# Optimization experiments

Measured on AMD Instinct MI355X. Metric: run time of the kernel, lower is better.

Reference implementation:

```python
import jax, jax.numpy as jnp
from jax import lax
import numpy as np

EPS = 1e-06


def _box_filter(x, radius):
    # Depthwise box mean with zero padding (matches F.conv2d padding=radius),
    # implemented separably: O(r) per pixel instead of O(r^2).
    C = x.shape[1]
    k = 2 * radius + 1
    dn = ('NCHW', 'OIHW', 'NCHW')
    kern_h = jnp.ones((C, 1, k, 1), x.dtype)
    kern_w = jnp.ones((C, 1, 1, k), x.dtype) / (k * k)
    y = lax.conv_general_dilated(x, kern_h, (1, 1), [(radius, radius), (0, 0)],
                                 feature_group_count=C, dimension_numbers=dn)
    return lax.conv_general_dilated(y, kern_w, (1, 1), [(0, 0), (radius, radius)],
                                    feature_group_count=C, dimension_numbers=dn)


def setup_inputs() -> dict:
    key = jax.random.key(0)
    k1, k2 = jax.random.split(key)
    I = jax.random.uniform(k1, (8, 1, 1024, 1024), dtype=jnp.float32)
    p = jax.random.uniform(k2, (8, 3, 1024, 1024), dtype=jnp.float32)
    return {"I": I, "p": p, "radius": 3}


def reference(I, p, radius):
    mean_I = _box_filter(I, radius)            # (B,1,H,W)
    mean_p = _box_filter(p, radius)            # (B,3,H,W)
    mean_Ip = _box_filter(I * p, radius)
    mean_II = _box_filter(I * I, radius)
    cov_Ip = mean_Ip - mean_I * mean_p
    var_I = mean_II - mean_I * mean_I
    a = cov_Ip / (var_I + EPS)
    b = mean_p - a * mean_I
    mean_a = _box_filter(a, radius)
    mean_b = _box_filter(b, radius)
    q = mean_a * I + mean_b
    return jnp.clip(q, 0.0, 1.0)
```

## Files before the change

kernel.cpp:

```cpp
#include <hip/hip_runtime.h>


#define TPB   128
#define OUTW  116
#define SEGH  64
#define HW    1024
#define GW    134
#define EPSF  1e-6f
#define INV49 (1.0f/49.0f)

struct GFState {
    float4 rr[8];
    float ra0[8], rb0[8], ra1[8], rb1[8], ra2[8], rb2[8];
    float sI, sII, sp0, sp1, sp2, sq0, sq1, sq2;
    float t6a0, t6b0, t6a1, t6b1, t6a2, t6b2;
    float4 cur[4];
};

template<int JB>
__device__ __forceinline__ void halfStep(
    GFState& S, int j0, int Yb, int x_in, bool xok, int xc, int tid,
    const float* __restrict__ Ip, const float* __restrict__ P0,
    const float* __restrict__ P1, const float* __restrict__ P2,
    float* __restrict__ Q0, float* __restrict__ Q1, float* __restrict__ Q2,
    float4 (*cs8A)[GW], float4 (*cs8B)[GW],
    float4 (*cs6A)[GW], float2 (*cs6B)[GW],
    bool dostore, bool dopref)
{
    float Io[4];
    #pragma unroll
    for (int u = 0; u < 4; ++u) Io[u] = S.rr[(JB+u+2)&7].x;

    #pragma unroll
    for (int u = 0; u < 4; ++u) {
        const float4 c = S.cur[u];
        const float4 o = S.rr[(JB+u+1)&7];
        S.sI  += c.x - o.x;
        S.sII += c.x*c.x - o.x*o.x;
        S.sp0 += c.y - o.y;  S.sq0 += c.x*c.y - o.x*o.y;
        S.sp1 += c.z - o.z;  S.sq1 += c.x*c.z - o.x*o.z;
        S.sp2 += c.w - o.w;  S.sq2 += c.x*c.w - o.x*o.w;
        S.rr[(JB+u)&7] = c;
        cs8A[(JB+u)&3][tid+3] = make_float4(S.sI,  S.sII, S.sp0, S.sp1);
        cs8B[(JB+u)&3][tid+3] = make_float4(S.sp2, S.sq0, S.sq1, S.sq2);
    }
    __syncthreads();

    #pragma unroll
    for (int u = 0; u < 4; ++u) {
        const int ls = (JB+u)&3;
        float4 A = make_float4(0.f,0.f,0.f,0.f);
        float4 B = make_float4(0.f,0.f,0.f,0.f);
        #pragma unroll
        for (int d = 0; d < 7; ++d) {
            float4 a = cs8A[ls][tid+d];
            float4 b = cs8B[ls][tid+d];
            A.x += a.x; A.y += a.y; A.z += a.z; A.w += a.w;
            B.x += b.x; B.y += b.y; B.z += b.z; B.w += b.w;
        }
        const int  yc   = Yb + j0 + u - 3;
        const bool abok = xok && ((unsigned)yc < HW);
        const float mi  = A.x*INV49, mii = A.y*INV49;
        const float rv  = __builtin_amdgcn_rcpf(mii - mi*mi + EPSF);
        float a0,b0,a1,b1,a2,b2, mp, mq, a, b;
        mp = A.z*INV49; mq = B.y*INV49;
        a = (mq - mi*mp)*rv; b = fmaf(-a, mi, mp);
        a0 = abok ? a : 0.f; b0 = abok ? b : 0.f;
        mp = A.w*INV49; mq = B.z*INV49;
        a = (mq - mi*mp)*rv; b = fmaf(-a, mi, mp);
        a1 = abok ? a : 0.f; b1 = abok ? b : 0.f;
        mp = B.x*INV49; mq = B.w*INV49;
        a = (mq - mi*mp)*rv; b = fmaf(-a, mi, mp);
        a2 = abok ? a : 0.f; b2 = abok ? b : 0.f;

        const int as = (JB+u)&7, al = (JB+u+1)&7;
        S.t6a0 += a0 - S.ra0[al]; S.ra0[as] = a0;
        S.t6b0 += b0 - S.rb0[al]; S.rb0[as] = b0;
        S.t6a1 += a1 - S.ra1[al]; S.ra1[as] = a1;
        S.t6b1 += b1 - S.rb1[al]; S.rb1[as] = b1;
        S.t6a2 += a2 - S.ra2[al]; S.ra2[as] = a2;
        S.t6b2 += b2 - S.rb2[al]; S.rb2[as] = b2;
        cs6A[ls][tid+3] = make_float4(S.t6a0, S.t6b0, S.t6a1, S.t6b1);
        cs6B[ls][tid+3] = make_float2(S.t6a2, S.t6b2);
    }
    __syncthreads();

    if (dopref) {
        #pragma unroll
        for (int u = 0; u < 4; ++u) {
            const int y  = Yb + j0 + 4 + u;
            const bool ok = xok && ((unsigned)y < HW);
            const int yy = min(max(y, 0), HW-1);
            const size_t off = (size_t)yy*HW + xc;
            float v0 = Ip[off], v1 = P0[off], v2 = P1[off], v3 = P2[off];
            float4 v;
            v.x = ok ? v0 : 0.f; v.y = ok ? v1 : 0.f;
            v.z = ok ? v2 : 0.f; v.w = ok ? v3 : 0.f;
            S.cur[u] = v;
        }
    }

    if (dostore) {
        const bool sok = (tid >= 6) && (tid < 122) && (x_in < HW);
        #pragma unroll
        for (int u = 0; u < 4; ++u) {
            const int ls = (JB+u)&3;
            float4 A6 = make_float4(0.f,0.f,0.f,0.f);
            float2 B6 = make_float2(0.f,0.f);
            #pragma unroll
            for (int d = 0; d < 7; ++d) {
                float4 a = cs6A[ls][tid+d];
                float2 b = cs6B[ls][tid+d];
                A6.x += a.x; A6.y += a.y; A6.z += a.z; A6.w += a.w;
                B6.x += b.x; B6.y += b.y;
            }
            const int o = Yb + j0 + u - 6;
            const size_t ooff = (size_t)o*HW + x_in;
            float q;
            q = fmaf(A6.x*INV49, Io[u], A6.y*INV49);
            q = fminf(fmaxf(q, 0.f), 1.f); if (sok) Q0[ooff] = q;
            q = fmaf(A6.z*INV49, Io[u], A6.w*INV49);
            q = fminf(fmaxf(q, 0.f), 1.f); if (sok) Q1[ooff] = q;
            q = fmaf(B6.x*INV49, Io[u], B6.y*INV49);
            q = fminf(fmaxf(q, 0.f), 1.f); if (sok) Q2[ooff] = q;
        }
    }
}

__global__ __launch_bounds__(TPB, 2) void gf_kernel(
    const float* __restrict__ I, const float* __restrict__ P,
    float* __restrict__ Q)
{
    __shared__ float4 cs8A[4][GW];
    __shared__ float4 cs8B[4][GW];
    __shared__ float4 cs6A[4][GW];
    __shared__ float2 cs6B[4][GW];

    const int s   = blockIdx.x;
    const int seg = blockIdx.y;
    const int b   = blockIdx.z;
    const int tid = threadIdx.x;

    const int X0   = s*OUTW - 6;
    const int Yb   = seg*SEGH - 6;
    const int x_in = X0 + tid;
    const bool xok = (unsigned)x_in < HW;
    const int  xc  = min(max(x_in, 0), HW-1);

    const float* Ip = I + (size_t)b*HW*HW;
    const float* P0 = P + ((size_t)b*3 + 0)*HW*HW;
    const float* P1 = P + ((size_t)b*3 + 1)*HW*HW;
    const float* P2 = P + ((size_t)b*3 + 2)*HW*HW;
    float* Q0 = Q + ((size_t)b*3 + 0)*HW*HW;
    float* Q1 = Q + ((size_t)b*3 + 1)*HW*HW;
    float* Q2 = Q + ((size_t)b*3 + 2)*HW*HW;

    {
        float4* zA = (float4*)cs8A;
        float4* zB = (float4*)cs8B;
        float4* zC = (float4*)cs6A;
        float2* zD = (float2*)cs6B;
        const float4 z4 = make_float4(0.f,0.f,0.f,0.f);
        const float2 z2 = make_float2(0.f,0.f);
        for (int i = tid; i < 4*GW; i += TPB) {
            zA[i] = z4; zB[i] = z4; zC[i] = z4; zD[i] = z2;
        }
    }

    GFState S;
    S.sI=S.sII=S.sp0=S.sp1=S.sp2=S.sq0=S.sq1=S.sq2=0.f;
    S.t6a0=S.t6b0=S.t6a1=S.t6b1=S.t6a2=S.t6b2=0.f;
    #pragma unroll
    for (int i = 0; i < 8; ++i) {
        S.rr[i] = make_float4(0.f,0.f,0.f,0.f);
        S.ra0[i]=S.rb0[i]=S.ra1[i]=S.rb1[i]=S.ra2[i]=S.rb2[i]=0.f;
    }
    #pragma unroll
    for (int u = 0; u < 4; ++u) {
        const int y = Yb + u;
        const bool ok = xok && ((unsigned)y < HW);
        const int yy = min(max(y, 0), HW-1);
        const size_t off = (size_t)yy*HW + xc;
        float v0 = Ip[off], v1 = P0[off], v2 = P1[off], v3 = P2[off];
        float4 v;
        v.x = ok ? v0 : 0.f; v.y = ok ? v1 : 0.f;
        v.z = ok ? v2 : 0.f; v.w = ok ? v3 : 0.f;
        S.cur[u] = v;
    }

    __syncthreads();

    for (int m = 0; m < 9; ++m) {
        const int j0 = m*8;
        halfStep<0>(S, j0,   Yb, x_in, xok, xc, tid, Ip, P0, P1, P2,
                    Q0, Q1, Q2, cs8A, cs8B, cs6A, cs6B,
                    (j0   >= 12), true);
        halfStep<4>(S, j0+4, Yb, x_in, xok, xc, tid, Ip, P0, P1, P2,
                    Q0, Q1, Q2, cs8A, cs8B, cs6A, cs6B,
                    (j0+4 >= 12), true);
    }
    halfStep<0>(S, 72, Yb, x_in, xok, xc, tid, Ip, P0, P1, P2,
                Q0, Q1, Q2, cs8A, cs8B, cs6A, cs6B,
                true, false);
}

extern "C" void kernel_launch(void* const* d_in, const int* in_sizes, int n_in,
                              void* d_out, int out_size, void* d_ws, size_t ws_size,
                              hipStream_t stream) {
    const float* I = (const float*)d_in[0];
    const float* P = (const float*)d_in[1];
    float* Q = (float*)d_out;

    dim3 grid(9, 16, 8);
    gf_kernel<<<grid, TPB, 0, stream>>>(I, P, Q);
}
```

Before: 285.8 us.

## Use single-wavefront blocks with two columns per thread and no barriers

Shrinks the block to one 64-thread wavefront, each thread handling two adjacent columns with float2 global loads and stores. Cross-thread sharing through LDS then relies on wavefront lockstep, with only compiler memory fences instead of __syncthreads. The leaving row is reloaded from global memory rather than kept in a register ring, trading extra (likely cached) loads for fewer registers. Correctness depends on implicit wave-synchronous LDS ordering, with LDS buffers double-buffered by row parity.

After: 323.4 us. +13.1%, slower.

```diff
diff --git a/kernel.cpp b/kernel.cpp
--- a/kernel.cpp
+++ b/kernel.cpp
@@ -1,151 +1,195 @@
 #include <hip/hip_runtime.h>
 
 
-#define TPB   128
+typedef float v4 __attribute__((ext_vector_type(4)));
+typedef float v2 __attribute__((ext_vector_type(2)));
+
+#define TPB   64
 #define OUTW  116
 #define SEGH  64
 #define HW    1024
-#define GW    134
+#define NIDX  68
 #define EPSF  1e-6f
 #define INV49 (1.0f/49.0f)
 
-struct GFState {
-    float4 rr[8];
-    float ra0[8], rb0[8], ra1[8], rb1[8], ra2[8], rb2[8];
-    float sI, sII, sp0, sp1, sp2, sq0, sq1, sq2;
-    float t6a0, t6b0, t6a1, t6b1, t6a2, t6b2;
-    float4 cur[4];
+struct St {
+    v4 s14[2], s58[2];
+    v4 t64[2]; v2 t62[2];
+    v4 rab4[8][2]; v2 rab2[8][2];
+    v4 ent[2][2];
+    v4 lv[2], lvN[2];
+    v2 Io, IoN;
 };
 
-template<int JB>
-__device__ __forceinline__ void halfStep(
-    GFState& S, int j0, int Yb, int x_in, bool xok, int xc, int tid,
+template<int U>
+__device__ __forceinline__ void rowStep(
+    St& S, const int r, const int Yb, const int t, const int xc2,
+    const bool ok0, const bool ok1, const bool sok, const int x0,
     const float* __restrict__ Ip, const float* __restrict__ P0,
     const float* __restrict__ P1, const float* __restrict__ P2,
     float* __restrict__ Q0, float* __restrict__ Q1, float* __restrict__ Q2,
-    float4 (*cs8A)[GW], float4 (*cs8B)[GW],
-    float4 (*cs6A)[GW], float2 (*cs6B)[GW],
-    bool dostore, bool dopref)
+    v4 (* __restrict__ c8)[2][2][NIDX],
+    v4 (* __restrict__ c6A)[2][NIDX],
+    v2 (* __restrict__ c6B)[2][NIDX])
 {
-    float Io[4];
+    constexpr int SU = U & 1;
+    constexpr int WS = U;
+    constexpr int LS = (U + 1) & 7;
+
     #pragma unroll
-    for (int u = 0; u < 4; ++u) Io[u] = S.rr[(JB+u+2)&7].x;
-
-    #pragma unroll
-    for (int u = 0; u < 4; ++u) {
-        const float4 c = S.cur[u];
-        const float4 o = S.rr[(JB+u+1)&7];
-        S.sI  += c.x - o.x;
-        S.sII += c.x*c.x - o.x*o.x;
-        S.sp0 += c.y - o.y;  S.sq0 += c.x*c.y - o.x*o.y;
-        S.sp1 += c.z - o.z;  S.sq1 += c.x*c.z - o.x*o.z;
-        S.sp2 += c.w - o.w;  S.sq2 += c.x*c.w - o.x*o.w;
-        S.rr[(JB+u)&7] = c;
-        cs8A[(JB+u)&3][tid+3] = make_float4(S.sI,  S.sII, S.sp0, S.sp1);
-        cs8B[(JB+u)&3][tid+3] = make_float4(S.sp2, S.sq0, S.sq1, S.sq2);
-    }
-    __syncthreads();
-
-    #pragma unroll
-    for (int u = 0; u < 4; ++u) {
-        const int ls = (JB+u)&3;
-        float4 A = make_float4(0.f,0.f,0.f,0.f);
-        float4 B = make_float4(0.f,0.f,0.f,0.f);
+    for (int c = 0; c < 2; ++c) {
+        const v4 cE = S.ent[SU][c];
+        const v4 L  = S.lv[c];
+        v4 d14, d58;
+        d14.x = cE.x - L.x;
+        d14.y = cE.x*cE.x - L.x*L.x;
+        d14.z = cE.y - L.y;
+        d14.w = cE.z - L.z;
+        d58.x = cE.w - L.w;
+        d58.y = cE.x*cE.y - L.x*L.y;
+        d58.z = cE.x*cE.z - L.x*L.z;
+        d58.w = cE.x*cE.w - L.x*L.w;
+        S.s14[c] += d14;
+        S.s58[c] += d58;
+        c8[SU][c][0][t+2] = S.s14[c];
+        c8[SU][c][1][t+2] = S.s58[c];
+    }
+    asm volatile("" ::: "memory");
+
+    {
+        const v4 e14_1 = c8[SU][0][0][t+1], e14_2 = c8[SU][0][0][t+2],
+                 e14_3 = c8[SU][0][0][t+3], e14_4 = c8[SU][0][0][t+4];
+        const v4 o14_0 = c8[SU][1][0][t+0], o14_1 = c8[SU][1][0][t+1],
+                 o14_2 = c8[SU][1][0][t+2], o14_3 = c8[SU][1][0][t+3];
+        const v4 w14 = (e14_1 + e14_2 + e14_3) + (o14_1 + o14_2 + o14_3);
+        v4 W14[2]; W14[0] = w14 + o14_0; W14[1] = w14 + e14_4;
+
+        const v4 e58_1 = c8[SU][0][1][t+1], e58_2 = c8[SU][0][1][t+2],
+                 e58_3 = c8[SU][0][1][t+3], e58_4 = c8[SU][0][1][t+4];
+        const v4 o58_0 = c8[SU][1][1][t+0], o58_1 = c8[SU][1][1][t+1],
+                 o58_2 = c8[SU][1][1][t+2], o58_3 = c8[SU][1][1][t+3];
+        const v4 w58 = (e58_1 + e58_2 + e58_3) + (o58_1 + o58_2 + o58_3);
+        v4 W58[2]; W58[0] = w58 + o58_0; W58[1] = w58 + e58_4;
+
+        const int  yc   = Yb + r - 3;
+        const bool ycok = (unsigned)yc < HW;
+        const bool okc[2] = {ok0, ok1};
         #pragma unroll
-        for (int d = 0; d < 7; ++d) {
-            float4 a = cs8A[ls][tid+d];
-            float4 b = cs8B[ls][tid+d];
-            A.x += a.x; A.y += a.y; A.z += a.z; A.w += a.w;
-            B.x += b.x; B.y += b.y; B.z += b.z; B.w += b.w;
-        }
-        const int  yc   = Yb + j0 + u - 3;
-        const bool abok = xok && ((unsigned)yc < HW);
-        const float mi  = A.x*INV49, mii = A.y*INV49;
-        const float rv  = __builtin_amdgcn_rcpf(mii - mi*mi + EPSF);
-        float a0,b0,a1,b1,a2,b2, mp, mq, a, b;
-        mp = A.z*INV49; mq = B.y*INV49;
-        a = (mq - mi*mp)*rv; b = fmaf(-a, mi, mp);
-        a0 = abok ? a : 0.f; b0 = abok ? b : 0.f;
-        mp = A.w*INV49; mq = B.z*INV49;
-        a = (mq - mi*mp)*rv; b = fmaf(-a, mi, mp);
-        a1 = abok ? a : 0.f; b1 = abok ? b : 0.f;
-        mp = B.x*INV49; mq = B.w*INV49;
-        a = (mq - mi*mp)*rv; b = fmaf(-a, mi, mp);
-        a2 = abok ? a : 0.f; b2 = abok ? b : 0.f;
-
-        const int as = (JB+u)&7, al = (JB+u+1)&7;
-        S.t6a0 += a0 - S.ra0[al]; S.ra0[as] = a0;
-        S.t6b0 += b0 - S.rb0[al]; S.rb0[as] = b0;
-        S.t6a1 += a1 - S.ra1[al]; S.ra1[as] = a1;
-        S.t6b1 += b1 - S.rb1[al]; S.rb1[as] = b1;
-        S.t6a2 += a2 - S.ra2[al]; S.ra2[as] = a2;
-        S.t6b2 += b2 - S.rb2[al]; S.rb2[as] = b2;
-        cs6A[ls][tid+3] = make_float4(S.t6a0, S.t6b0, S.t6a1, S.t6b1);
-        cs6B[ls][tid+3] = make_float2(S.t6a2, S.t6b2);
-    }
-    __syncthreads();
-
-    if (dopref) {
-        #pragma unroll
-        for (int u = 0; u < 4; ++u) {
-            const int y  = Yb + j0 + 4 + u;
-            const bool ok = xok && ((unsigned)y < HW);
-            const int yy = min(max(y, 0), HW-1);
-            const size_t off = (size_t)yy*HW + xc;
-            float v0 = Ip[off], v1 = P0[off], v2 = P1[off], v3 = P2[off];
-            float4 v;
-            v.x = ok ? v0 : 0.f; v.y = ok ? v1 : 0.f;
-            v.z = ok ? v2 : 0.f; v.w = ok ? v3 : 0.f;
-            S.cur[u] = v;
-        }
-    }
-
-    if (dostore) {
-        const bool sok = (tid >= 6) && (tid < 122) && (x_in < HW);
-        #pragma unroll
-        for (int u = 0; u < 4; ++u) {
-            const int ls = (JB+u)&3;
-            float4 A6 = make_float4(0.f,0.f,0.f,0.f);
-            float2 B6 = make_float2(0.f,0.f);
-            #pragma unroll
-            for (int d = 0; d < 7; ++d) {
-                float4 a = cs6A[ls][tid+d];
-                float2 b = cs6B[ls][tid+d];
-                A6.x += a.x; A6.y += a.y; A6.z += a.z; A6.w += a.w;
-                B6.x += b.x; B6.y += b.y;
-            }
-            const int o = Yb + j0 + u - 6;
-            const size_t ooff = (size_t)o*HW + x_in;
-            float q;
-            q = fmaf(A6.x*INV49, Io[u], A6.y*INV49);
-            q = fminf(fmaxf(q, 0.f), 1.f); if (sok) Q0[ooff] = q;
-            q = fmaf(A6.z*INV49, Io[u], A6.w*INV49);
-            q = fminf(fmaxf(q, 0.f), 1.f); if (sok) Q1[ooff] = q;
-            q = fmaf(B6.x*INV49, Io[u], B6.y*INV49);
-            q = fminf(fmaxf(q, 0.f), 1.f); if (sok) Q2[ooff] = q;
-        }
-    }
+        for (int c = 0; c < 2; ++c) {
+            const v4 A = W14[c], B = W58[c];
+            const float mi  = A.x * INV49;
+            const float mii = A.y * INV49;
+            const float rv  = __builtin_amdgcn_rcpf(mii - mi*mi + EPSF);
+            const bool abok = ycok && okc[c];
+            const float mp0 = A.z*INV49, mp1 = A.w*INV49, mp2 = B.x*INV49;
+            const float a0 = (B.y*INV49 - mi*mp0)*rv;
+            const float a1 = (B.z*INV49 - mi*mp1)*rv;
+            const float a2 = (B.w*INV49 - mi*mp2)*rv;
+            const float b0 = fmaf(-a0, mi, mp0);
+            const float b1 = fmaf(-a1, mi, mp1);
+            const float b2 = fmaf(-a2, mi, mp2);
+            v4 ab4; ab4.x = abok?a0:0.f; ab4.y = abok?b0:0.f;
+                    ab4.z = abok?a1:0.f; ab4.w = abok?b1:0.f;
+            v2 ab2; ab2.x = abok?a2:0.f; ab2.y = abok?b2:0.f;
+            S.t64[c] += ab4 - S.rab4[LS][c];  S.rab4[WS][c] = ab4;
+            S.t62[c] += ab2 - S.rab2[LS][c];  S.rab2[WS][c] = ab2;
+            c6A[SU][c][t+2] = S.t64[c];
+            c6B[SU][c][t+2] = S.t62[c];
+        }
+    }
+    asm volatile("" ::: "memory");
+
+    {
+        const int yE = Yb + r + 2;
+        if ((unsigned)yE < HW) {
+            const size_t ro = (size_t)yE * HW + xc2;
+            const v2 vI = *(const v2*)(Ip + ro);
+            const v2 va = *(const v2*)(P0 + ro);
+            const v2 vb = *(const v2*)(P1 + ro);
+            const v2 vc = *(const v2*)(P2 + ro);
+            v4 E0, E1;
+            E0.x = ok0?vI.x:0.f; E0.y = ok0?va.x:0.f; E0.z = ok0?vb.x:0.f; E0.w = ok0?vc.x:0.f;
+            E1.x = ok1?vI.y:0.f; E1.y = ok1?va.y:0.f; E1.z = ok1?vb.y:0.f; E1.w = ok1?vc.y:0.f;
+            S.ent[SU][0] = E0; S.ent[SU][1] = E1;
+        } else {
+            const v4 z = {0.f,0.f,0.f,0.f};
+            S.ent[SU][0] = z; S.ent[SU][1] = z;
+        }
+        const int yL = Yb + r - 6;
+        if (r >= 6 && (unsigned)yL < HW) {
+            const size_t ro = (size_t)yL * HW + xc2;
+            const v2 vI = *(const v2*)(Ip + ro);
+            const v2 va = *(const v2*)(P0 + ro);
+            const v2 vb = *(const v2*)(P1 + ro);
+            const v2 vc = *(const v2*)(P2 + ro);
+            v4 L0, L1;
+            L0.x = ok0?vI.x:0.f; L0.y = ok0?va.x:0.f; L0.z = ok0?vb.x:0.f; L0.w = ok0?vc.x:0.f;
+            L1.x = ok1?vI.y:0.f; L1.y = ok1?va.y:0.f; L1.z = ok1?vb.y:0.f; L1.w = ok1?vc.y:0.f;
+            S.lvN[0] = L0; S.lvN[1] = L1;
+        } else {
+            const v4 z = {0.f,0.f,0.f,0.f};
+            S.lvN[0] = z; S.lvN[1] = z;
+        }
+        const int yO = Yb + r - 5;
+        if ((unsigned)yO < HW) {
+            const size_t ro = (size_t)yO * HW + xc2;
+            const v2 vio = *(const v2*)(Ip + ro);
+            S.IoN.x = ok0?vio.x:0.f; S.IoN.y = ok1?vio.y:0.f;
+        } else { S.IoN.x = 0.f; S.IoN.y = 0.f; }
+    }
+
+    if ((unsigned)(r - 12) <= 63u) {
+        const v4 eA1 = c6A[SU][0][t+1], eA2 = c6A[SU][0][t+2],
+                 eA3 = c6A[SU][0][t+3], eA4 = c6A[SU][0][t+4];
+        const v4 oA0 = c6A[SU][1][t+0], oA1 = c6A[SU][1][t+1],
+                 oA2 = c6A[SU][1][t+2], oA3 = c6A[SU][1][t+3];
+        const v2 eB1 = c6B[SU][0][t+1], eB2 = c6B[SU][0][t+2],
+                 eB3 = c6B[SU][0][t+3], eB4 = c6B[SU][0][t+4];
+        const v2 oB0 = c6B[SU][1][t+0], oB1 = c6B[SU][1][t+1],
+                 oB2 = c6B[SU][1][t+2], oB3 = c6B[SU][1][t+3];
+        const v4 wA = (eA1+eA2+eA3) + (oA1+oA2+oA3);
+        const v2 wB = (eB1+eB2+eB3) + (oB1+oB2+oB3);
+        const v4 A0 = wA + oA0, A1 = wA + eA4;
+        const v2 B0 = wB + oB0, B1 = wB + eB4;
+        if (sok) {
+            const int o = Yb + r - 6;
+            const size_t ob = (size_t)o * HW + x0;
+            v2 q;
+            q.x = fminf(fmaxf(fmaf(A0.x*INV49, S.Io.x, A0.y*INV49), 0.f), 1.f);
+            q.y = fminf(fmaxf(fmaf(A1.x*INV49, S.Io.y, A1.y*INV49), 0.f), 1.f);
+            *(v2*)(Q0 + ob) = q;
+            q.x = fminf(fmaxf(fmaf(A0.z*INV49, S.Io.x, A0.w*INV49), 0.f), 1.f);
+            q.y = fminf(fmaxf(fmaf(A1.z*INV49, S.Io.y, A1.w*INV49), 0.f), 1.f);
+            *(v2*)(Q1 + ob) = q;
+            q.x = fminf(fmaxf(fmaf(B0.x*INV49, S.Io.x, B0.y*INV49), 0.f), 1.f);
+            q.y = fminf(fmaxf(fmaf(B1.x*INV49, S.Io.y, B1.y*INV49), 0.f), 1.f);
+            *(v2*)(Q2 + ob) = q;
+        }
+    }
+    S.lv[0] = S.lvN[0]; S.lv[1] = S.lvN[1];
+    S.Io = S.IoN;
 }
 
 __global__ __launch_bounds__(TPB, 2) void gf_kernel(
     const float* __restrict__ I, const float* __restrict__ P,
     float* __restrict__ Q)
 {
-    __shared__ float4 cs8A[4][GW];
-    __shared__ float4 cs8B[4][GW];
-    __shared__ float4 cs6A[4][GW];
-    __shared__ float2 cs6B[4][GW];
+    __shared__ v4 c8[2][2][2][NIDX];
+    __shared__ v4 c6A[2][2][NIDX];
+    __shared__ v2 c6B[2][2][NIDX];
 
     const int s   = blockIdx.x;
     const int seg = blockIdx.y;
     const int b   = blockIdx.z;
-    const int tid = threadIdx.x;
-
-    const int X0   = s*OUTW - 6;
-    const int Yb   = seg*SEGH - 6;
-    const int x_in = X0 + tid;
-    const bool xok = (unsigned)x_in < HW;
-    const int  xc  = min(max(x_in, 0), HW-1);
+    const int t   = threadIdx.x;
+
+    const int Yb = seg*SEGH - 6;
+    const int x0 = s*OUTW - 6 + 2*t;
+    const int x1 = x0 + 1;
+    const bool ok0 = (unsigned)x0 < HW;
+    const bool ok1 = (unsigned)x1 < HW;
+    const int  xc2 = min(max(x0, 0), HW-2);
+    const bool sok = (t >= 3) && (t <= 60) && ok0 && ok1;
 
     const float* Ip = I + (size_t)b*HW*HW;
     const float* P0 = P + ((size_t)b*3 + 0)*HW*HW;
@@ -156,52 +200,64 @@
     float* Q2 = Q + ((size_t)b*3 + 2)*HW*HW;
 
     {
-        float4* zA = (float4*)cs8A;
-        float4* zB = (float4*)cs8B;
-        float4* zC = (float4*)cs6A;
-        float2* zD = (float2*)cs6B;
-        const float4 z4 = make_float4(0.f,0.f,0.f,0.f);
-        const float2 z2 = make_float2(0.f,0.f);
-        for (int i = tid; i < 4*GW; i += TPB) {
-            zA[i] = z4; zB[i] = z4; zC[i] = z4; zD[i] = z2;
-        }
-    }
-
-    GFState S;
-    S.sI=S.sII=S.sp0=S.sp1=S.sp2=S.sq0=S.sq1=S.sq2=0.f;
-    S.t6a0=S.t6b0=S.t6a1=S.t6b1=S.t6a2=S.t6b2=0.f;
-    #pragma unroll
-    for (int i = 0; i < 8; ++i) {
-        S.rr[i] = make_float4(0.f,0.f,0.f,0.f);
-        S.ra0[i]=S.rb0[i]=S.ra1[i]=S.rb1[i]=S.ra2[i]=S.rb2[i]=0.f;
-    }
-    #pragma unroll
-    for (int u = 0; u < 4; ++u) {
-        const int y = Yb + u;
-        const bool ok = xok && ((unsigned)y < HW);
-        const int yy = min(max(y, 0), HW-1);
-        const size_t off = (size_t)yy*HW + xc;
-        float v0 = Ip[off], v1 = P0[off], v2 = P1[off], v3 = P2[off];
-        float4 v;
-        v.x = ok ? v0 : 0.f; v.y = ok ? v1 : 0.f;
-        v.z = ok ? v2 : 0.f; v.w = ok ? v3 : 0.f;
-        S.cur[u] = v;
-    }
-
+        const v4 z4 = {0.f,0.f,0.f,0.f};
+        const v2 z2 = {0.f,0.f};
+        v4* a = (v4*)c8;
+        #pragma unroll 2
+        for (int i = t; i < 2*2*2*NIDX; i += TPB) a[i] = z4;
+        v4* bb = (v4*)c6A;
+        for (int i = t; i < 2*2*NIDX; i += TPB) bb[i] = z4;
+        v2* cc = (v2*)c6B;
+        for (int i = t; i < 2*2*NIDX; i += TPB) cc[i] = z2;
+    }
+
+    St S;
+    {
+        const v4 z4 = {0.f,0.f,0.f,0.f};
+        const v2 z2 = {0.f,0.f};
+        #pragma unroll
+        for (int c = 0; c < 2; ++c) {
+            S.s14[c] = z4; S.s58[c] = z4; S.t64[c] = z4; S.t62[c] = z2;
+            S.lv[c] = z4; S.lvN[c] = z4;
+            #pragma unroll
+            for (int i = 0; i < 8; ++i) { S.rab4[i][c] = z4; S.rab2[i][c] = z2; }
+        }
+        S.Io = z2; S.IoN = z2;
+        #pragma unroll
+        for (int pr = 0; pr < 2; ++pr) {
+            const int yE = Yb + pr;
+            if ((unsigned)yE < HW) {
+                const size_t ro = (size_t)yE * HW + xc2;
+                const v2 vI = *(const v2*)(Ip + ro);
+                const v2 va = *(const v2*)(P0 + ro);
+                const v2 vb = *(const v2*)(P1 + ro);
+                const v2 vc = *(const v2*)(P2 + ro);
+                v4 E0, E1;
+                E0.x = ok0?vI.x:0.f; E0.y = ok0?va.x:0.f; E0.z = ok0?vb.x:0.f; E0.w = ok0?vc.x:0.f;
+                E1.x = ok1?vI.y:0.f; E1.y = ok1?va.y:0.f; E1.z = ok1?vb.y:0.f; E1.w = ok1?vc.y:0.f;
+                S.ent[pr][0] = E0; S.ent[pr][1] = E1;
+            } else {
+                S.ent[pr][0] = z4; S.ent[pr][1] = z4;
+            }
+        }
+    }
     __syncthreads();
 
     for (int m = 0; m < 9; ++m) {
-        const int j0 = m*8;
-        halfStep<0>(S, j0,   Yb, x_in, xok, xc, tid, Ip, P0, P1, P2,
-                    Q0, Q1, Q2, cs8A, cs8B, cs6A, cs6B,
-                    (j0   >= 12), true);
-        halfStep<4>(S, j0+4, Yb, x_in, xok, xc, tid, Ip, P0, P1, P2,
-                    Q0, Q1, Q2, cs8A, cs8B, cs6A, cs6B,
-                    (j0+4 >= 12), true);
-    }
-    halfStep<0>(S, 72, Yb, x_in, xok, xc, tid, Ip, P0, P1, P2,
-                Q0, Q1, Q2, cs8A, cs8B, cs6A, cs6B,
-                true, false);
+        const int r0 = m*8;
+        rowStep<0>(S, r0+0, Yb, t, xc2, ok0, ok1, sok, x0, Ip,P0,P1,P2, Q0,Q1,Q2, c8,c6A,c6B);
+        rowStep<1>(S, r0+1, Yb, t, xc2, ok0, ok1, sok, x0, Ip,P0,P1,P2, Q0,Q1,Q2, c8,c6A,c6B);
+        rowStep<2>(S, r0+2, Yb, t, xc2, ok0, ok1, sok, x0, Ip,P0,P1,P2, Q0,Q1,Q2, c8,c6A,c6B);
+        rowStep<3>(S, r0+3, Yb, t, xc2, ok0, ok1, sok, x0, Ip,P0,P1,P2, Q0,Q1,Q2, c8,c6A,c6B);
+        rowStep<4>(S, r0+4, Yb, t, xc2, ok0, ok1, sok, x0, Ip,P0,P1,P2, Q0,Q1,Q2, c8,c6A,c6B);
+        rowStep<5>(S, r0+5, Yb, t, xc2, ok0, ok1, sok, x0, Ip,P0,P1,P2, Q0,Q1,Q2, c8,c6A,c6B);
+        rowStep<6>(S, r0+6, Yb, t, xc2, ok0, ok1, sok, x0, Ip,P0,P1,P2, Q0,Q1,Q2, c8,c6A,c6B);
+        rowStep<7>(S, r0+7, Yb, t, xc2, ok0, ok1, sok, x0, Ip,P0,P1,P2, Q0,Q1,Q2, c8,c6A,c6B);
+    }
+    rowStep<0>(S, 72, Yb, t, xc2, ok0, ok1, sok, x0, Ip,P0,P1,P2, Q0,Q1,Q2, c8,c6A,c6B);
+    rowStep<1>(S, 73, Yb, t, xc2, ok0, ok1, sok, x0, Ip,P0,P1,P2, Q0,Q1,Q2, c8,c6A,c6B);
+    rowStep<2>(S, 74, Yb, t, xc2, ok0, ok1, sok, x0, Ip,P0,P1,P2, Q0,Q1,Q2, c8,c6A,c6B);
+    rowStep<3>(S, 75, Yb, t, xc2, ok0, ok1, sok, x0, Ip,P0,P1,P2, Q0,Q1,Q2, c8,c6A,c6B);
 }
 
 extern "C" void kernel_launch(void* const* d_in, const int* in_sizes, int n_in,
```
